# Kernel optimization log

Measured on AMD Instinct MI355X. Metric: run time of the kernel, lower is better.

## Reference

```python
import jax, jax.numpy as jnp
import numpy as np

EPS_ATTN = 1e-6
EPS_LN = 1e-5


def _layer_norm(x, g, b):
    m = jnp.mean(x, axis=-1, keepdims=True)
    v = jnp.mean((x - m) ** 2, axis=-1, keepdims=True)
    return (x - m) * jax.lax.rsqrt(v + EPS_LN) * g + b


def _linear_attention(q, k, v):
    # q,k,v: [N, L/S, H, D]; elu feature map (+1 keeps values positive)
    q = jax.nn.elu(q) + 1.0
    k = jax.nn.elu(k) + 1.0
    s_len = v.shape[1]
    v = v / s_len
    kv = jnp.einsum('nshd,nshv->nhdv', k, v)            # [N,H,D,D]
    z = 1.0 / (jnp.einsum('nlhd,nhd->nlh', q, k.sum(axis=1)) + EPS_ATTN)
    out = jnp.einsum('nlhd,nhdv->nlhv', q, kv) * z[..., None] * s_len
    return out


def setup_inputs() -> dict:
    key = jax.random.key(0)
    ks = jax.random.split(key, 8)
    N, L, S, H, D = 4, 4096, 4096, 8, 64
    sc = 0.05
    return {
        'x': jax.random.normal(ks[0], (N, L, H, D), jnp.float32),
        'source': jax.random.normal(ks[1], (N, S, H, D), jnp.float32),
        'wq': jax.random.normal(ks[2], (D, D), jnp.float32) * sc,
        'wk': jax.random.normal(ks[3], (D, D), jnp.float32) * sc,
        'wv': jax.random.normal(ks[4], (D, D), jnp.float32) * sc,
        'wmerge': jax.random.normal(ks[5], (D, D), jnp.float32) * sc,
        'w1': jax.random.normal(ks[6], (2 * D, 2 * D), jnp.float32) * sc,
        'w2': jax.random.normal(ks[7], (D, 2 * D), jnp.float32) * sc,
        'g1': jnp.ones((D,), jnp.float32),
        'b1': jnp.zeros((D,), jnp.float32),
        'g2': jnp.ones((D,), jnp.float32),
        'b2': jnp.zeros((D,), jnp.float32),
    }


def reference(x, source, wq, wk, wv, wmerge, w1, w2, g1, b1, g2, b2):
    # projections (torch Linear: y = x @ W.T), applied on last dim D=d_model
    q = jnp.einsum('nlhd,ed->nlhe', x, wq)
    k = jnp.einsum('nshd,ed->nshe', source, wk)
    v = jnp.einsum('nshd,ed->nshe', source, wv)
    message = _linear_attention(q, k, v)                # [N,L,H,D]
    message = jnp.einsum('nlhd,ed->nlhe', message, wmerge)
    message = _layer_norm(message, g1, b1)
    h = jnp.concatenate([x, message], axis=-1)          # [N,L,H,2D]
    h = jax.nn.relu(jnp.einsum('nlhd,ed->nlhe', h, w1))
    h = jnp.einsum('nlhd,ed->nlhe', h, w2)              # [N,L,H,D]
    h = _layer_norm(h, g2, b2)
    return x + h
```

## Files before the change

### kernel.cpp

```cpp
#include <hip/hip_runtime.h>
#include <cstdint>

#define NB 4
#define LL 4096
#define SS 4096
#define HH 8
#define DD 64
#define NHC (NB*HH)

typedef unsigned short ushort_t;
typedef __bf16 bf16x8 __attribute__((ext_vector_type(8)));
typedef float f32x4 __attribute__((ext_vector_type(4)));
typedef unsigned short u16x8 __attribute__((ext_vector_type(8)));
typedef unsigned short u16x4 __attribute__((ext_vector_type(4)));

__device__ __forceinline__ float bf2f(unsigned short u) {
    union { unsigned int i; float f; } v; v.i = ((unsigned int)u) << 16; return v.f;
}
__device__ __forceinline__ unsigned short f2bf(float f) {
    union { float ff; unsigned int i; } v; v.ff = f;
    unsigned int x = v.i;
    x += 0x7fffu + ((x >> 16) & 1u);
    return (unsigned short)(x >> 16);
}
__device__ __forceinline__ bool input_is_bf16(const void* g1) {
    return ((const unsigned short*)g1)[0] == 0x3F80u;
}

template<bool BF16>
__device__ __forceinline__ float ldgf(const void* p, size_t i) {
    if constexpr (BF16) return bf2f(((const unsigned short*)p)[i]);
    else                return ((const float*)p)[i];
}
template<bool BF16>
__device__ __forceinline__ u16x8 ld8(const void* p, size_t i) {
    if constexpr (BF16) {
        return *reinterpret_cast<const u16x8*>((const unsigned short*)p + i);
    } else {
        const float* f = (const float*)p + i;
        u16x8 o;
        #pragma unroll
        for (int j = 0; j < 8; ++j) o[j] = f2bf(f[j]);
        return o;
    }
}
__device__ __forceinline__ bf16x8 ldsA(const ushort_t* p) {
    return *reinterpret_cast<const bf16x8*>(p);
}
#define MFMA16(a,b,c) __builtin_amdgcn_mfma_f32_16x16x32_bf16(a,b,c,0,0,0)

template<bool BF16, int LC>
__device__ __forceinline__ void stage_w(const void* g, size_t goff, ushort_t* dst,
                                        int rows, int dstride, int tid) {
    int total8 = (rows << LC) >> 3;
    for (int i8 = tid; i8 < total8; i8 += 256) {
        int i = i8 << 3;
        int r = i >> LC, c = i & ((1 << LC) - 1);
        *reinterpret_cast<u16x8*>(dst + r * dstride + c) = ld8<BF16>(g, goff + i);
    }
}

__device__ __forceinline__ void red16(float v[4]) {
    #pragma unroll
    for (int m = 1; m < 16; m <<= 1) {
        #pragma unroll
        for (int r = 0; r < 4; ++r) v[r] += __shfl_xor(v[r], m);
    }
}

template<bool BF16>
__device__ void kv_body(const void* __restrict__ src, const void* __restrict__ wk,
                        const void* __restrict__ wv, float* __restrict__ kvg,
                        float* __restrict__ ksumg,
                        ushort_t* S, ushort_t* KT, ushort_t* VT)
{
    const int tid = threadIdx.x;
    const int lane = tid & 63, w = tid >> 6;
    const int lg = lane >> 4, l15 = lane & 15;
    const int bid = blockIdx.x;
    const int nh = bid >> 5, ch = bid & 31;
    const int n = nh >> 3, h = nh & 7;
    const int s0 = ch * 128;
    const f32x4 z4 = {0.f, 0.f, 0.f, 0.f};

    stage_w<BF16, 6>(wk, 0, KT, 64, 136, tid);
    stage_w<BF16, 6>(wv, 0, VT, 64, 136, tid);
    for (int i = tid; i < 128 * 8; i += 256) {
        int r = i >> 3, c8 = (i & 7) << 3;
        size_t gb = ((size_t)((size_t)n * SS + (s0 + r)) * HH + h) * DD + c8;
        *reinterpret_cast<u16x8*>(S + r * 72 + c8) = ld8<BF16>(src, gb);
    }
    __syncthreads();

    bf16x8 wkf[2][4], wvf[2][4];
    #pragma unroll
    for (int ks = 0; ks < 2; ++ks)
        #pragma unroll
        for (int nt = 0; nt < 4; ++nt) {
            wkf[ks][nt] = ldsA(KT + (nt * 16 + l15) * 136 + ks * 32 + lg * 8);
            wvf[ks][nt] = ldsA(VT + (nt * 16 + l15) * 136 + ks * 32 + lg * 8);
        }
    __syncthreads();

    float ksp[4] = {0.f, 0.f, 0.f, 0.f};
    #pragma unroll
    for (int mtt = 0; mtt < 2; ++mtt) {
        const int rowA = w * 32 + mtt * 16;
        bf16x8 af[2];
        #pragma unroll
        for (int ks = 0; ks < 2; ++ks)
            af[ks] = ldsA(S + (rowA + l15) * 72 + ks * 32 + lg * 8);
        f32x4 ka[4], va[4];
        #pragma unroll
        for (int nt = 0; nt < 4; ++nt) { ka[nt] = z4; va[nt] = z4; }
        #pragma unroll
        for (int ks = 0; ks < 2; ++ks)
            #pragma unroll
            for (int nt = 0; nt < 4; ++nt) {
                ka[nt] = MFMA16(af[ks], wkf[ks][nt], ka[nt]);
                va[nt] = MFMA16(af[ks], wvf[ks][nt], va[nt]);
            }
        #pragma unroll
        for (int nt = 0; nt < 4; ++nt) {
            u16x4 kp, vp;
            #pragma unroll
            for (int r = 0; r < 4; ++r) {
                float kvl = ka[nt][r];
                kvl = kvl > 0.f ? kvl + 1.f : __expf(kvl);
                ksp[nt] += kvl;
                kp[r] = f2bf(kvl);
                vp[r] = f2bf(va[nt][r]);
            }
            const int dcol = nt * 16 + l15;
            *reinterpret_cast<u16x4*>(KT + dcol * 136 + rowA + lg * 4) = kp;
            *reinterpret_cast<u16x4*>(VT + dcol * 136 + rowA + lg * 4) = vp;
        }
    }
    __syncthreads();

    f32x4 kvacc[4];
    #pragma unroll
    for (int nt = 0; nt < 4; ++nt) kvacc[nt] = z4;
    #pragma unroll
    for (int ks = 0; ks < 4; ++ks) {
        bf16x8 akv = ldsA(KT + (w * 16 + l15) * 136 + ks * 32 + lg * 8);
        #pragma unroll
        for (int nt = 0; nt < 4; ++nt) {
            bf16x8 bkv = ldsA(VT + (nt * 16 + l15) * 136 + ks * 32 + lg * 8);
            kvacc[nt] = MFMA16(akv, bkv, kvacc[nt]);
        }
    }

    float* kvo = kvg + (size_t)nh * DD * DD;
    #pragma unroll
    for (int nt = 0; nt < 4; ++nt)
        #pragma unroll
        for (int r = 0; r < 4; ++r)
            atomicAdd(&kvo[(w * 16 + lg * 4 + r) * DD + nt * 16 + l15], kvacc[nt][r]);
    #pragma unroll
    for (int m = 16; m < 64; m <<= 1)
        #pragma unroll
        for (int nt = 0; nt < 4; ++nt) ksp[nt] += __shfl_xor(ksp[nt], m);
    if (lane < 16) {
        #pragma unroll
        for (int nt = 0; nt < 4; ++nt)
            atomicAdd(&ksumg[nh * DD + nt * 16 + lane], ksp[nt]);
    }
}

__global__ __launch_bounds__(256, 3) void kv_kernel(
    const void* __restrict__ src, const void* __restrict__ wk, const void* __restrict__ wv,
    const void* __restrict__ g1, float* __restrict__ kvg, float* __restrict__ ksumg)
{
    __shared__ ushort_t S[128 * 72];
    __shared__ ushort_t KT[64 * 136];
    __shared__ ushort_t VT[64 * 136];
    if (input_is_bf16(g1)) kv_body<true >(src, wk, wv, kvg, ksumg, S, KT, VT);
    else                   kv_body<false>(src, wk, wv, kvg, ksumg, S, KT, VT);
}

template<bool BF16>
__device__ void main_body(const void* __restrict__ x,
                          const void* __restrict__ wq, const void* __restrict__ wm,
                          const void* __restrict__ w1, const void* __restrict__ w2,
                          const void* __restrict__ g1, const void* __restrict__ b1,
                          const void* __restrict__ g2, const void* __restrict__ b2,
                          const float* __restrict__ kvg, const float* __restrict__ ksumg,
                          void* __restrict__ outp,
                          ushort_t* w1s, ushort_t* kvs, ushort_t* B0, ushort_t* B1,
                          ushort_t* B2)
{
    const int tid = threadIdx.x;
    const int lane = tid & 63, w = tid >> 6;
    const int lg = lane >> 4, l15 = lane & 15;
    const int bid = blockIdx.x;
    const int nh = bid >> 4, ch = bid & 15;
    const int n = nh >> 3, h = nh & 7;
    const int rowA = w * 16;
    const f32x4 z4 = {0.f, 0.f, 0.f, 0.f};

    auto ldx = [&](int t, u16x8 xv[2]) {
        #pragma unroll
        for (int p = 0; p < 2; ++p) {
            int r16 = p * 8 + (lane >> 3), c8 = (lane & 7) << 3;
            size_t gb = ((size_t)((size_t)n * LL + (ch * 256 + t * 64 + rowA + r16)) * HH + h) * DD + c8;
            xv[p] = ld8<BF16>(x, gb);
        }
    };

    u16x8 xv[2];
    ldx(0, xv);

    stage_w<BF16, 6>(wq, 0, B0, 64, 72, tid);
    stage_w<BF16, 6>(wm, 0, B1, 64, 72, tid);
    stage_w<BF16, 7>(w2, 0, w1s, 64, 136, tid);
    for (int i = tid; i < 4096; i += 256) {
        int d = i >> 6, e = i & 63;
        B2[d * 72 + e] = f2bf(kvg[(size_t)nh * 4096 + i]);
    }
    __syncthreads();

    bf16x8 wqf[2][4], w2f[4][4];
    #pragma unroll
    for (int ks = 0; ks < 2; ++ks)
        #pragma unroll
        for (int nt = 0; nt < 4; ++nt)
            wqf[ks][nt] = ldsA(B0 + (nt * 16 + l15) * 72 + ks * 32 + lg * 8);
    #pragma unroll
    for (int ks = 0; ks < 4; ++ks)
        #pragma unroll
        for (int nt = 0; nt < 4; ++nt)
            w2f[ks][nt] = ldsA(w1s + (nt * 16 + l15) * 136 + ks * 32 + lg * 8);
    {
        bf16x8 akv[2];
        #pragma unroll
        for (int ks = 0; ks < 2; ++ks)
            akv[ks] = ldsA(B2 + (w * 16 + l15) * 72 + ks * 32 + lg * 8);
        f32x4 km[4];
        #pragma unroll
        for (int nt = 0; nt < 4; ++nt) km[nt] = z4;
        #pragma unroll
        for (int ks = 0; ks < 2; ++ks)
            #pragma unroll
            for (int nt = 0; nt < 4; ++nt) {
                bf16x8 bwm = ldsA(B1 + (nt * 16 + l15) * 72 + ks * 32 + lg * 8);
                km[nt] = MFMA16(akv[ks], bwm, km[nt]);
            }
        #pragma unroll
        for (int nt = 0; nt < 4; ++nt)
            #pragma unroll
            for (int r = 0; r < 4; ++r)
                kvs[(nt * 16 + l15) * 72 + w * 16 + lg * 4 + r] = f2bf(km[nt][r]);
    }
    __syncthreads();

    stage_w<BF16, 7>(w1, 0, w1s, 128, 136, tid);
    bf16x8 kvmf[2][4];
    #pragma unroll
    for (int ks = 0; ks < 2; ++ks)
        #pragma unroll
        for (int nt = 0; nt < 4; ++nt)
            kvmf[ks][nt] = ldsA(kvs + (nt * 16 + l15) * 72 + ks * 32 + lg * 8);
    float g1r[4], b1r[4], g2r[4], b2r[4], ksr[4];
    #pragma unroll
    for (int nt = 0; nt < 4; ++nt) {
        int c = nt * 16 + l15;
        g1r[nt] = ldgf<BF16>(g1, c); b1r[nt] = ldgf<BF16>(b1, c);
        g2r[nt] = ldgf<BF16>(g2, c); b2r[nt] = ldgf<BF16>(b2, c);
        ksr[nt] = ksumg[nh * 64 + c];
    }
    __syncthreads();

    for (int t = 0; t < 4; ++t) {
        const int l0 = ch * 256 + t * 64;

        #pragma unroll
        for (int p = 0; p < 2; ++p) {
            int r16 = p * 8 + (lane >> 3), c8 = (lane & 7) << 3;
            *reinterpret_cast<u16x8*>(B0 + (rowA + r16) * 72 + c8) = xv[p];
        }
        u16x8 xn[2];
        if (t < 3) ldx(t + 1, xn);

        bf16x8 af[2];
        #pragma unroll
        for (int ks = 0; ks < 2; ++ks)
            af[ks] = ldsA(B0 + (rowA + l15) * 72 + ks * 32 + lg * 8);
        f32x4 qa[4];
        #pragma unroll
        for (int nt = 0; nt < 4; ++nt) qa[nt] = z4;
        __builtin_amdgcn_s_setprio(1);
        #pragma unroll
        for (int ks = 0; ks < 2; ++ks)
            #pragma unroll
            for (int nt = 0; nt < 4; ++nt)
                qa[nt] = MFMA16(af[ks], wqf[ks][nt], qa[nt]);
        __builtin_amdgcn_s_setprio(0);
        float zp[4] = {0.f, 0.f, 0.f, 0.f};
        #pragma unroll
        for (int nt = 0; nt < 4; ++nt)
            #pragma unroll
            for (int r = 0; r < 4; ++r) {
                float v = qa[nt][r];
                v = v > 0.f ? v + 1.f : __expf(v);
                zp[r] += v * ksr[nt];
                B1[(rowA + lg * 4 + r) * 72 + nt * 16 + l15] = f2bf(v);
            }
        red16(zp);
        float zr[4];
        #pragma unroll
        for (int r = 0; r < 4; ++r) zr[r] = 1.f / (zp[r] + 1e-6f);

        #pragma unroll
        for (int ks = 0; ks < 2; ++ks)
            af[ks] = ldsA(B1 + (rowA + l15) * 72 + ks * 32 + lg * 8);
        f32x4 ma[4];
        #pragma unroll
        for (int nt = 0; nt < 4; ++nt) ma[nt] = z4;
        __builtin_amdgcn_s_setprio(1);
        #pragma unroll
        for (int ks = 0; ks < 2; ++ks)
            #pragma unroll
            for (int nt = 0; nt < 4; ++nt)
                ma[nt] = MFMA16(af[ks], kvmf[ks][nt], ma[nt]);
        __builtin_amdgcn_s_setprio(0);
        #pragma unroll
        for (int nt = 0; nt < 4; ++nt)
            #pragma unroll
            for (int r = 0; r < 4; ++r) ma[nt][r] *= zr[r];

        float s1[4] = {0.f,0.f,0.f,0.f}, s2[4] = {0.f,0.f,0.f,0.f};
        #pragma unroll
        for (int nt = 0; nt < 4; ++nt)
            #pragma unroll
            for (int r = 0; r < 4; ++r) {
                float v = ma[nt][r]; s1[r] += v; s2[r] += v * v;
            }
        red16(s1); red16(s2);
        #pragma unroll
        for (int r = 0; r < 4; ++r) {
            float mu = s1[r] * 0.015625f;
            float var = s2[r] * 0.015625f - mu * mu;
            s1[r] = mu; s2[r] = rsqrtf(var + 1e-5f);
        }
        #pragma unroll
        for (int nt = 0; nt < 4; ++nt)
            #pragma unroll
            for (int r = 0; r < 4; ++r)
                B1[(rowA + lg * 4 + r) * 72 + nt * 16 + l15] =
                    f2bf((ma[nt][r] - s1[r]) * s2[r] * g1r[nt] + b1r[nt]);

        f32x4 ha[4];
        #pragma unroll
        for (int nt = 0; nt < 4; ++nt) ha[nt] = z4;
        #pragma unroll
        for (int half = 0; half < 2; ++half) {
            f32x4 ta[4];
            #pragma unroll
            for (int nt = 0; nt < 4; ++nt) ta[nt] = z4;
            __builtin_amdgcn_s_setprio(1);
            #pragma unroll
            for (int ks = 0; ks < 4; ++ks) {
                const ushort_t* bp = (ks < 2) ? B0 : B1;
                bf16x8 a1 = ldsA(bp + (rowA + l15) * 72 + (ks & 1) * 32 + lg * 8);
                #pragma unroll
                for (int nt = 0; nt < 4; ++nt) {
                    bf16x8 bw = ldsA(w1s + (half * 64 + nt * 16 + l15) * 136 + ks * 32 + lg * 8);
                    ta[nt] = MFMA16(a1, bw, ta[nt]);
                }
            }
            __builtin_amdgcn_s_setprio(0);
            #pragma unroll
            for (int nt = 0; nt < 4; ++nt)
                #pragma unroll
                for (int r = 0; r < 4; ++r)
                    B2[(rowA + lg * 4 + r) * 72 + nt * 16 + l15] =
                        f2bf(fmaxf(ta[nt][r], 0.f));
            __builtin_amdgcn_s_setprio(1);
            #pragma unroll
            for (int k2 = 0; k2 < 2; ++k2) {
                bf16x8 a2 = ldsA(B2 + (rowA + l15) * 72 + k2 * 32 + lg * 8);
                #pragma unroll
                for (int nt = 0; nt < 4; ++nt)
                    ha[nt] = MFMA16(a2, w2f[half * 2 + k2][nt], ha[nt]);
            }
            __builtin_amdgcn_s_setprio(0);
        }

        float t1[4] = {0.f,0.f,0.f,0.f}, t2[4] = {0.f,0.f,0.f,0.f};
        #pragma unroll
        for (int nt = 0; nt < 4; ++nt)
            #pragma unroll
            for (int r = 0; r < 4; ++r) {
                float v = ha[nt][r]; t1[r] += v; t2[r] += v * v;
            }
        red16(t1); red16(t2);
        #pragma unroll
        for (int r = 0; r < 4; ++r) {
            float mu = t1[r] * 0.015625f;
            float var = t2[r] * 0.015625f - mu * mu;
            t1[r] = mu; t2[r] = rsqrtf(var + 1e-5f);
        }
        #pragma unroll
        for (int nt = 0; nt < 4; ++nt)
            #pragma unroll
            for (int r = 0; r < 4; ++r) {
                float xv2 = bf2f(B0[(rowA + lg * 4 + r) * 72 + nt * 16 + l15]);
                float ov = xv2 + (ha[nt][r] - t1[r]) * t2[r] * g2r[nt] + b2r[nt];
                B1[(rowA + lg * 4 + r) * 72 + nt * 16 + l15] = f2bf(ov);
            }

        #pragma unroll
        for (int p = 0; p < 2; ++p) {
            int r16 = p * 8 + (lane >> 3), c8 = (lane & 7) << 3;
            size_t gb = ((size_t)((size_t)n * LL + (l0 + rowA + r16)) * HH + h) * DD + c8;
            u16x8 v = *reinterpret_cast<const u16x8*>(B1 + (rowA + r16) * 72 + c8);
            if constexpr (BF16) {
                *reinterpret_cast<u16x8*>((unsigned short*)outp + gb) = v;
            } else {
                float* fo = (float*)outp + gb;
                #pragma unroll
                for (int j = 0; j < 8; ++j) fo[j] = bf2f(v[j]);
            }
        }

        if (t < 3) { xv[0] = xn[0]; xv[1] = xn[1]; }
    }
}

__global__ __launch_bounds__(256, 2) void main_kernel(
    const void* __restrict__ x,
    const void* __restrict__ wq, const void* __restrict__ wm,
    const void* __restrict__ w1, const void* __restrict__ w2,
    const void* __restrict__ g1, const void* __restrict__ b1,
    const void* __restrict__ g2, const void* __restrict__ b2,
    const float* __restrict__ kvg, const float* __restrict__ ksumg,
    void* __restrict__ outp)
{
    __shared__ ushort_t w1s[128 * 136];
    __shared__ ushort_t kvs[64 * 72];
    __shared__ ushort_t B0[64 * 72];
    __shared__ ushort_t B1[64 * 72];
    __shared__ ushort_t B2[64 * 72];
    if (input_is_bf16(g1))
        main_body<true >(x, wq, wm, w1, w2, g1, b1, g2, b2, kvg, ksumg, outp,
                         w1s, kvs, B0, B1, B2);
    else
        main_body<false>(x, wq, wm, w1, w2, g1, b1, g2, b2, kvg, ksumg, outp,
                         w1s, kvs, B0, B1, B2);
}

extern "C" void kernel_launch(void* const* d_in, const int* in_sizes, int n_in,
                              void* d_out, int out_size, void* d_ws, size_t ws_size,
                              hipStream_t stream) {
    const void* x   = d_in[0];
    const void* src = d_in[1];
    const void* wq  = d_in[2];
    const void* wk  = d_in[3];
    const void* wv  = d_in[4];
    const void* wm  = d_in[5];
    const void* w1  = d_in[6];
    const void* w2  = d_in[7];
    const void* g1  = d_in[8];
    const void* b1  = d_in[9];
    const void* g2  = d_in[10];
    const void* b2  = d_in[11];

    float* kvg   = (float*)d_ws;
    float* ksumg = kvg + (size_t)NHC * DD * DD;

    hipMemsetAsync(d_ws, 0, ((size_t)NHC * DD * DD + NHC * DD) * sizeof(float), stream);
    kv_kernel<<<NHC * 32, 256, 0, stream>>>(src, wk, wv, g1, kvg, ksumg);
    main_kernel<<<NHC * 16, 256, 0, stream>>>(x, wq, wm, w1, w2, g1, b1, g2, b2,
                                              kvg, ksumg, d_out);
}
```

Baseline: 171.0 us.

## Replace KV atomics and memset with per-chunk partials reduced in main kernel

The KV kernel now handles 256 source rows per block in two staged halves, which halves the grid. Instead of using atomicAdd into a zeroed buffer, each block writes its partial KV matrix and key-sum to its own workspace slot. The main kernel sums the 16 partials while staging. This removes the memset launch and the atomic contention, at the cost of extra workspace traffic and a reduction in the main kernel's prologue. It also vectorizes the fp32 loads and stores, switches to the native bf16 convert, and adds setprio around the MFMA blocks.

```diff
diff --git a/kernel.cpp b/kernel.cpp
--- a/kernel.cpp
+++ b/kernel.cpp
@@ -7,6 +7,7 @@
 #define HH 8
 #define DD 64
 #define NHC (NB*HH)
+#define KVCH 16
 
 typedef unsigned short ushort_t;
 typedef __bf16 bf16x8 __attribute__((ext_vector_type(8)));
@@ -18,10 +19,7 @@
     union { unsigned int i; float f; } v; v.i = ((unsigned int)u) << 16; return v.f;
 }
 __device__ __forceinline__ unsigned short f2bf(float f) {
-    union { float ff; unsigned int i; } v; v.ff = f;
-    unsigned int x = v.i;
-    x += 0x7fffu + ((x >> 16) & 1u);
-    return (unsigned short)(x >> 16);
+    union { __bf16 b; unsigned short u; } v; v.b = (__bf16)f; return v.u;
 }
 __device__ __forceinline__ bool input_is_bf16(const void* g1) {
     return ((const unsigned short*)g1)[0] == 0x3F80u;
@@ -37,10 +35,11 @@
     if constexpr (BF16) {
         return *reinterpret_cast<const u16x8*>((const unsigned short*)p + i);
     } else {
-        const float* f = (const float*)p + i;
+        const f32x4* f4 = reinterpret_cast<const f32x4*>((const float*)p + i);
+        f32x4 a = f4[0], b = f4[1];
         u16x8 o;
         #pragma unroll
-        for (int j = 0; j < 8; ++j) o[j] = f2bf(f[j]);
+        for (int j = 0; j < 4; ++j) { o[j] = f2bf(a[j]); o[4 + j] = f2bf(b[j]); }
         return o;
     }
 }
@@ -68,25 +67,25 @@
     }
 }
 
-template<bool BF16>
+template<bool BF16, bool PART>
 __device__ void kv_body(const void* __restrict__ src, const void* __restrict__ wk,
                         const void* __restrict__ wv, float* __restrict__ kvg,
                         float* __restrict__ ksumg,
-                        ushort_t* S, ushort_t* KT, ushort_t* VT)
+                        ushort_t* S, ushort_t* KT, ushort_t* VT, float* KS)
 {
     const int tid = threadIdx.x;
     const int lane = tid & 63, w = tid >> 6;
     const int lg = lane >> 4, l15 = lane & 15;
     const int bid = blockIdx.x;
-    const int nh = bid >> 5, ch = bid & 31;
+    const int nh = bid >> 4, ch = bid & 15;
     const int n = nh >> 3, h = nh & 7;
-    const int s0 = ch * 128;
+    const int s0 = ch * 256;
     const f32x4 z4 = {0.f, 0.f, 0.f, 0.f};
 
     stage_w<BF16, 6>(wk, 0, KT, 64, 136, tid);
     stage_w<BF16, 6>(wv, 0, VT, 64, 136, tid);
-    for (int i = tid; i < 128 * 8; i += 256) {
-        int r = i >> 3, c8 = (i & 7) << 3;
+    for (int i8 = tid; i8 < 1024; i8 += 256) {
+        int r = i8 >> 3, c8 = (i8 & 7) << 3;
         size_t gb = ((size_t)((size_t)n * SS + (s0 + r)) * HH + h) * DD + c8;
         *reinterpret_cast<u16x8*>(S + r * 72 + c8) = ld8<BF16>(src, gb);
     }
@@ -102,84 +101,115 @@
         }
     __syncthreads();
 
+    f32x4 kvacc[4];
+    #pragma unroll
+    for (int nt = 0; nt < 4; ++nt) kvacc[nt] = z4;
     float ksp[4] = {0.f, 0.f, 0.f, 0.f};
-    #pragma unroll
-    for (int mtt = 0; mtt < 2; ++mtt) {
-        const int rowA = w * 32 + mtt * 16;
-        bf16x8 af[2];
-        #pragma unroll
-        for (int ks = 0; ks < 2; ++ks)
-            af[ks] = ldsA(S + (rowA + l15) * 72 + ks * 32 + lg * 8);
-        f32x4 ka[4], va[4];
-        #pragma unroll
-        for (int nt = 0; nt < 4; ++nt) { ka[nt] = z4; va[nt] = z4; }
-        #pragma unroll
-        for (int ks = 0; ks < 2; ++ks)
+
+    for (int st = 0; st < 2; ++st) {
+        #pragma unroll
+        for (int mtt = 0; mtt < 2; ++mtt) {
+            const int rowA = w * 32 + mtt * 16;
+            bf16x8 af[2];
+            #pragma unroll
+            for (int ks = 0; ks < 2; ++ks)
+                af[ks] = ldsA(S + (rowA + l15) * 72 + ks * 32 + lg * 8);
+            f32x4 ka[4], va[4];
+            #pragma unroll
+            for (int nt = 0; nt < 4; ++nt) { ka[nt] = z4; va[nt] = z4; }
+            __builtin_amdgcn_s_setprio(1);
+            #pragma unroll
+            for (int ks = 0; ks < 2; ++ks)
+                #pragma unroll
+                for (int nt = 0; nt < 4; ++nt) {
+                    ka[nt] = MFMA16(af[ks], wkf[ks][nt], ka[nt]);
+                    va[nt] = MFMA16(af[ks], wvf[ks][nt], va[nt]);
+                }
+            __builtin_amdgcn_s_setprio(0);
             #pragma unroll
             for (int nt = 0; nt < 4; ++nt) {
-                ka[nt] = MFMA16(af[ks], wkf[ks][nt], ka[nt]);
-                va[nt] = MFMA16(af[ks], wvf[ks][nt], va[nt]);
-            }
-        #pragma unroll
-        for (int nt = 0; nt < 4; ++nt) {
-            u16x4 kp, vp;
-            #pragma unroll
-            for (int r = 0; r < 4; ++r) {
-                float kvl = ka[nt][r];
-                kvl = kvl > 0.f ? kvl + 1.f : __expf(kvl);
-                ksp[nt] += kvl;
-                kp[r] = f2bf(kvl);
-                vp[r] = f2bf(va[nt][r]);
-            }
-            const int dcol = nt * 16 + l15;
-            *reinterpret_cast<u16x4*>(KT + dcol * 136 + rowA + lg * 4) = kp;
-            *reinterpret_cast<u16x4*>(VT + dcol * 136 + rowA + lg * 4) = vp;
-        }
-    }
-    __syncthreads();
-
-    f32x4 kvacc[4];
-    #pragma unroll
-    for (int nt = 0; nt < 4; ++nt) kvacc[nt] = z4;
-    #pragma unroll
-    for (int ks = 0; ks < 4; ++ks) {
-        bf16x8 akv = ldsA(KT + (w * 16 + l15) * 136 + ks * 32 + lg * 8);
-        #pragma unroll
-        for (int nt = 0; nt < 4; ++nt) {
-            bf16x8 bkv = ldsA(VT + (nt * 16 + l15) * 136 + ks * 32 + lg * 8);
-            kvacc[nt] = MFMA16(akv, bkv, kvacc[nt]);
-        }
-    }
-
-    float* kvo = kvg + (size_t)nh * DD * DD;
-    #pragma unroll
-    for (int nt = 0; nt < 4; ++nt)
-        #pragma unroll
-        for (int r = 0; r < 4; ++r)
-            atomicAdd(&kvo[(w * 16 + lg * 4 + r) * DD + nt * 16 + l15], kvacc[nt][r]);
+                u16x4 kp, vp;
+                #pragma unroll
+                for (int r = 0; r < 4; ++r) {
+                    float kvl = ka[nt][r];
+                    kvl = kvl > 0.f ? kvl + 1.f : __expf(kvl);
+                    ksp[nt] += kvl;
+                    kp[r] = f2bf(kvl);
+                    vp[r] = f2bf(va[nt][r]);
+                }
+                const int dcol = nt * 16 + l15;
+                *reinterpret_cast<u16x4*>(KT + dcol * 136 + rowA + lg * 4) = kp;
+                *reinterpret_cast<u16x4*>(VT + dcol * 136 + rowA + lg * 4) = vp;
+            }
+        }
+        __syncthreads();
+
+        if (st == 0) {
+            for (int i8 = tid; i8 < 1024; i8 += 256) {
+                int r = i8 >> 3, c8 = (i8 & 7) << 3;
+                size_t gb = ((size_t)((size_t)n * SS + (s0 + 128 + r)) * HH + h) * DD + c8;
+                *reinterpret_cast<u16x8*>(S + r * 72 + c8) = ld8<BF16>(src, gb);
+            }
+        }
+        __builtin_amdgcn_s_setprio(1);
+        #pragma unroll
+        for (int ks = 0; ks < 4; ++ks) {
+            bf16x8 akv = ldsA(KT + (w * 16 + l15) * 136 + ks * 32 + lg * 8);
+            #pragma unroll
+            for (int nt = 0; nt < 4; ++nt) {
+                bf16x8 bkv = ldsA(VT + (nt * 16 + l15) * 136 + ks * 32 + lg * 8);
+                kvacc[nt] = MFMA16(akv, bkv, kvacc[nt]);
+            }
+        }
+        __builtin_amdgcn_s_setprio(0);
+        __syncthreads();
+    }
+
+    if constexpr (PART) {
+        float* kvo = kvg + (size_t)bid * 4096;
+        #pragma unroll
+        for (int nt = 0; nt < 4; ++nt)
+            #pragma unroll
+            for (int r = 0; r < 4; ++r)
+                kvo[(w * 16 + lg * 4 + r) * DD + nt * 16 + l15] = kvacc[nt][r];
+    } else {
+        float* kvo = kvg + (size_t)nh * 4096;
+        #pragma unroll
+        for (int nt = 0; nt < 4; ++nt)
+            #pragma unroll
+            for (int r = 0; r < 4; ++r)
+                atomicAdd(&kvo[(w * 16 + lg * 4 + r) * DD + nt * 16 + l15], kvacc[nt][r]);
+    }
     #pragma unroll
     for (int m = 16; m < 64; m <<= 1)
         #pragma unroll
         for (int nt = 0; nt < 4; ++nt) ksp[nt] += __shfl_xor(ksp[nt], m);
     if (lane < 16) {
         #pragma unroll
-        for (int nt = 0; nt < 4; ++nt)
-            atomicAdd(&ksumg[nh * DD + nt * 16 + lane], ksp[nt]);
-    }
-}
-
-__global__ __launch_bounds__(256, 3) void kv_kernel(
+        for (int nt = 0; nt < 4; ++nt) KS[w * 64 + nt * 16 + lane] = ksp[nt];
+    }
+    __syncthreads();
+    if (tid < 64) {
+        float s = KS[tid] + KS[64 + tid] + KS[128 + tid] + KS[192 + tid];
+        if constexpr (PART) ksumg[(size_t)bid * 64 + tid] = s;
+        else                atomicAdd(&ksumg[nh * 64 + tid], s);
+    }
+}
+
+template<bool PART>
+__global__ __launch_bounds__(256, 2) void kv_kernel(
     const void* __restrict__ src, const void* __restrict__ wk, const void* __restrict__ wv,
     const void* __restrict__ g1, float* __restrict__ kvg, float* __restrict__ ksumg)
 {
     __shared__ ushort_t S[128 * 72];
     __shared__ ushort_t KT[64 * 136];
     __shared__ ushort_t VT[64 * 136];
-    if (input_is_bf16(g1)) kv_body<true >(src, wk, wv, kvg, ksumg, S, KT, VT);
-    else                   kv_body<false>(src, wk, wv, kvg, ksumg, S, KT, VT);
-}
-
-template<bool BF16>
+    __shared__ float    KS[4 * 64];
+    if (input_is_bf16(g1)) kv_body<true , PART>(src, wk, wv, kvg, ksumg, S, KT, VT, KS);
+    else                   kv_body<false, PART>(src, wk, wv, kvg, ksumg, S, KT, VT, KS);
+}
+
+template<bool BF16, bool PART>
 __device__ void main_body(const void* __restrict__ x,
                           const void* __restrict__ wq, const void* __restrict__ wm,
                           const void* __restrict__ w1, const void* __restrict__ w2,
@@ -214,9 +244,24 @@
     stage_w<BF16, 6>(wq, 0, B0, 64, 72, tid);
     stage_w<BF16, 6>(wm, 0, B1, 64, 72, tid);
     stage_w<BF16, 7>(w2, 0, w1s, 64, 136, tid);
-    for (int i = tid; i < 4096; i += 256) {
-        int d = i >> 6, e = i & 63;
-        B2[d * 72 + e] = f2bf(kvg[(size_t)nh * 4096 + i]);
+    if constexpr (PART) {
+        for (int i4 = tid; i4 < 1024; i4 += 256) {
+            const float* base = kvg + (size_t)nh * KVCH * 4096 + i4 * 4;
+            f32x4 s = z4;
+            #pragma unroll
+            for (int c = 0; c < KVCH; ++c)
+                s += *reinterpret_cast<const f32x4*>(base + c * 4096);
+            int d = i4 >> 4, e4 = (i4 * 4) & 63;
+            u16x4 pk;
+            #pragma unroll
+            for (int j = 0; j < 4; ++j) pk[j] = f2bf(s[j]);
+            *reinterpret_cast<u16x4*>(B2 + d * 72 + e4) = pk;
+        }
+    } else {
+        for (int i = tid; i < 4096; i += 256) {
+            int d = i >> 6, e = i & 63;
+            B2[d * 72 + e] = f2bf(kvg[(size_t)nh * 4096 + i]);
+        }
     }
     __syncthreads();
 
@@ -267,7 +312,15 @@
         int c = nt * 16 + l15;
         g1r[nt] = ldgf<BF16>(g1, c); b1r[nt] = ldgf<BF16>(b1, c);
         g2r[nt] = ldgf<BF16>(g2, c); b2r[nt] = ldgf<BF16>(b2, c);
-        ksr[nt] = ksumg[nh * 64 + c];
+        if constexpr (PART) {
+            float s = 0.f;
+            #pragma unroll
+            for (int cc = 0; cc < KVCH; ++cc)
+                s += ksumg[((size_t)nh * KVCH + cc) * 64 + c];
+            ksr[nt] = s;
+        } else {
+            ksr[nt] = ksumg[nh * 64 + c];
+        }
     }
     __syncthreads();
 
@@ -419,8 +472,11 @@
                 *reinterpret_cast<u16x8*>((unsigned short*)outp + gb) = v;
             } else {
                 float* fo = (float*)outp + gb;
+                f32x4 lo, hi;
                 #pragma unroll
-                for (int j = 0; j < 8; ++j) fo[j] = bf2f(v[j]);
+                for (int j = 0; j < 4; ++j) { lo[j] = bf2f(v[j]); hi[j] = bf2f(v[4 + j]); }
+                *reinterpret_cast<f32x4*>(fo) = lo;
+                *reinterpret_cast<f32x4*>(fo + 4) = hi;
             }
         }
 
@@ -428,6 +484,7 @@
     }
 }
 
+template<bool PART>
 __global__ __launch_bounds__(256, 2) void main_kernel(
     const void* __restrict__ x,
     const void* __restrict__ wq, const void* __restrict__ wm,
@@ -443,11 +500,11 @@
     __shared__ ushort_t B1[64 * 72];
     __shared__ ushort_t B2[64 * 72];
     if (input_is_bf16(g1))
-        main_body<true >(x, wq, wm, w1, w2, g1, b1, g2, b2, kvg, ksumg, outp,
-                         w1s, kvs, B0, B1, B2);
+        main_body<true , PART>(x, wq, wm, w1, w2, g1, b1, g2, b2, kvg, ksumg, outp,
+                               w1s, kvs, B0, B1, B2);
     else
-        main_body<false>(x, wq, wm, w1, w2, g1, b1, g2, b2, kvg, ksumg, outp,
-                         w1s, kvs, B0, B1, B2);
+        main_body<false, PART>(x, wq, wm, w1, w2, g1, b1, g2, b2, kvg, ksumg, outp,
+                               w1s, kvs, B0, B1, B2);
 }
 
 extern "C" void kernel_launch(void* const* d_in, const int* in_sizes, int n_in,
@@ -466,11 +523,22 @@
     const void* g2  = d_in[10];
     const void* b2  = d_in[11];
 
-    float* kvg   = (float*)d_ws;
-    float* ksumg = kvg + (size_t)NHC * DD * DD;
-
-    hipMemsetAsync(d_ws, 0, ((size_t)NHC * DD * DD + NHC * DD) * sizeof(float), stream);
-    kv_kernel<<<NHC * 32, 256, 0, stream>>>(src, wk, wv, g1, kvg, ksumg);
-    main_kernel<<<NHC * 16, 256, 0, stream>>>(x, wq, wm, w1, w2, g1, b1, g2, b2,
-                                              kvg, ksumg, d_out);
-}
+    const size_t kv_elems   = (size_t)NHC * KVCH * 4096;
+    const size_t ksum_elems = (size_t)NHC * KVCH * 64;
+    const size_t need = (kv_elems + ksum_elems) * sizeof(float);
+
+    if (ws_size >= need) {
+        float* kvp = (float*)d_ws;
+        float* ksp = kvp + kv_elems;
+        kv_kernel<true ><<<NHC * KVCH, 256, 0, stream>>>(src, wk, wv, g1, kvp, ksp);
+        main_kernel<true ><<<NHC * 16, 256, 0, stream>>>(x, wq, wm, w1, w2, g1, b1,
+                                                         g2, b2, kvp, ksp, d_out);
+    } else {
+        float* kvg   = (float*)d_ws;
+        float* ksumg = kvg + (size_t)NHC * DD * DD;
+        hipMemsetAsync(d_ws, 0, ((size_t)NHC * DD * DD + NHC * DD) * sizeof(float), stream);
+        kv_kernel<false><<<NHC * KVCH, 256, 0, stream>>>(src, wk, wv, g1, kvg, ksumg);
+        main_kernel<false><<<NHC * 16, 256, 0, stream>>>(x, wq, wm, w1, w2, g1, b1,
+                                                         g2, b2, kvg, ksumg, d_out);
+    }
+}
```

Result: faster. 160.5 us (-6.2%).
